# Kernel tuning notes

Hardware: AMD Instinct MI355X
Metric: run time of the kernel (lower is better)

Reference implementation:

```python
import jax, jax.numpy as jnp
import numpy as np

DIM = 1024
H = 16
DH = DIM // H
NF = 64
EPS = 1e-6


def setup_inputs() -> dict:
    key = jax.random.key(0)
    ks = jax.random.split(key, 10)
    B, L = 4, 4096
    s = 1.0 / np.sqrt(DIM)
    x = jax.random.normal(ks[0], (B, L, DIM), dtype=jnp.float32)
    Wq = jax.random.normal(ks[1], (DIM, DIM), dtype=jnp.float32) * s
    Wk = jax.random.normal(ks[2], (DIM, DIM), dtype=jnp.float32) * s
    Wv = jax.random.normal(ks[3], (DIM, DIM), dtype=jnp.float32) * s
    Wo = jax.random.normal(ks[4], (DIM, DIM), dtype=jnp.float32) * s
    bq = jax.random.normal(ks[5], (DIM,), dtype=jnp.float32) * s
    bk = jax.random.normal(ks[6], (DIM,), dtype=jnp.float32) * s
    bv = jax.random.normal(ks[7], (DIM,), dtype=jnp.float32) * s
    bo = jax.random.normal(ks[8], (DIM,), dtype=jnp.float32) * s
    # random-feature buffer: [num_repeats=1, H, DH, NF]; use repeat 0
    Wrf = jax.random.normal(ks[9], (1, H, DH, NF), dtype=jnp.float32)
    return {"x": x, "Wq": Wq, "bq": bq, "Wk": Wk, "bk": bk, "Wv": Wv,
            "bv": bv, "Wo": Wo, "bo": bo, "Wrf": Wrf}


def reference(x, Wq, bq, Wk, bk, Wv, bv, Wo, bo, Wrf):
    B, L, _ = x.shape
    W0 = Wrf[0]  # [H, DH, NF]

    def split_heads(y):
        return y.reshape(B, L, H, DH).transpose(0, 2, 1, 3)  # [B,H,L,DH]

    q = split_heads(x @ Wq.T + bq)
    k = split_heads(x @ Wk.T + bk)
    v = split_heads(x @ Wv.T + bv)

    # key summary: logits [B,H,L,NF], softmax over flattened (L*NF)
    logits = jnp.einsum('bhld,hdf->bhlf', k, W0) \
             - 0.5 * jnp.sum(k * k, axis=-1, keepdims=True)
    alpha = jax.nn.softmax(logits.reshape(B, H, L * NF), axis=2)
    alpha = alpha.reshape(B, H, L, NF)
    N = jnp.einsum('bhlf,bhld->bhfd', alpha, v)  # [B,H,NF,DH]
    D = jnp.sum(alpha, axis=2)                   # [B,H,NF]

    # query feature map: per-position softmax over features
    phi = jax.nn.softmax(jnp.einsum('bhld,hdf->bhlf', q, W0), axis=-1)

    num = jnp.einsum('bhlf,bhfd->bhld', phi, N)
    den = jnp.einsum('bhlf,bhf->bhl', phi, D)
    out = num / (den[..., None] + EPS)

    ctx = out.transpose(0, 2, 1, 3).reshape(B, L, DIM)
    return ctx @ Wo.T + bo
```

## Files before the change

### kernel.cpp

```cpp
#include <hip/hip_runtime.h>
#include <hip/hip_bf16.h>

constexpr int NB   = 4;
constexpr int SL   = 4096;
constexpr int DIMC = 1024;
constexpr int NH   = 16;
constexpr int DHC  = 64;
constexpr int NFC  = 64;
constexpr int NCHK = 8;
constexpr int NCHQ = 32;
constexpr int LCQ  = SL / NCHQ;
constexpr float FEPS = 1e-6f;

typedef __attribute__((ext_vector_type(8))) short bf16x8_t;
typedef __attribute__((ext_vector_type(4))) float f32x4_t;
typedef __attribute__((ext_vector_type(4))) short s16x4_t;

__device__ __forceinline__ void load_lds_16B(const short* g, short* l) {
  __builtin_amdgcn_global_load_lds(
      (__attribute__((address_space(1))) void*)(g),
      (__attribute__((address_space(3))) void*)(l), 16, 0, 0);
}

__global__ __launch_bounds__(256) void cast_f32_to_bf16(
    const float* __restrict__ in, short* __restrict__ out, int n)
{
  const int i = (blockIdx.x * 256 + threadIdx.x) * 4;
  if (i >= n) return;
  const f32x4_t v = *(const f32x4_t*)(in + i);
  s16x4_t o;
#pragma unroll
  for (int j = 0; j < 4; j++) {
    __hip_bfloat16 h = __float2bfloat16(v[j]);
    o[j] = *(short*)&h;
  }
  *(s16x4_t*)(out + i) = o;
}

__global__ __launch_bounds__(256) void prep_w0t_kernel(
    const float* __restrict__ Wrf, short* __restrict__ Whi, short* __restrict__ Wlo)
{
  const int h = blockIdx.x;
  for (int t = threadIdx.x; t < 4096; t += 256) {
    const int f = t >> 6, dh = t & 63;
    const float w = Wrf[(size_t)h * 4096 + dh * 64 + f];
    __hip_bfloat16 hi = __float2bfloat16(w);
    const float rem = w - __bfloat162float(hi);
    __hip_bfloat16 lo = __float2bfloat16(rem);
    Whi[(size_t)h * 4096 + t] = *(short*)&hi;
    Wlo[(size_t)h * 4096 + t] = *(short*)&lo;
  }
}

template <int MODE>
__global__ __launch_bounds__(256) void gemm_lds_kernel(
    const short* __restrict__ A, const short* __restrict__ W,
    const float* __restrict__ bias, void* __restrict__ C0,
    void* __restrict__ C1, float* __restrict__ Ks)
{
  constexpr int K = 1024, N = 1024;
  const int lane = threadIdx.x & 63;
  const int wid  = threadIdx.x >> 6;
  const int sub  = lane & 15;
  const int quad = lane >> 4;
  const int wr   = (wid >> 1) * 64;
  const int wc   = (wid & 1) * 64;
  const int row0 = blockIdx.x * 128;
  const int col0 = blockIdx.y * 128;

  __shared__ short As[128 * 64];
  __shared__ short Bs[128 * 64];

  f32x4_t acc[4][4] = {};

  const int srow = lane >> 3;
  for (int k0 = 0; k0 < K; k0 += 64) {
#pragma unroll
    for (int t = 0; t < 4; t++) {
      const int R   = wid * 32 + t * 8;
      const int row = R + srow;
      const int c   = (lane & 7) ^ (row & 7);
      load_lds_16B(A + (size_t)(row0 + row) * K + k0 + c * 8, As + R * 64);
      load_lds_16B(W + (size_t)(col0 + row) * K + k0 + c * 8, Bs + R * 64);
    }
    __syncthreads();

    bf16x8_t a[2][4], b[2][4];
#pragma unroll
    for (int ks = 0; ks < 2; ks++) {
#pragma unroll
      for (int i = 0; i < 4; i++) {
        const int ra = wr + i * 16 + sub;
        a[ks][i] = *(const bf16x8_t*)(As + ra * 64 + (((ks * 4 + quad) ^ (ra & 7)) * 8));
        const int rb = wc + i * 16 + sub;
        b[ks][i] = *(const bf16x8_t*)(Bs + rb * 64 + (((ks * 4 + quad) ^ (rb & 7)) * 8));
      }
    }
#pragma unroll
    for (int ks = 0; ks < 2; ks++)
#pragma unroll
      for (int i = 0; i < 4; i++)
#pragma unroll
        for (int j = 0; j < 4; j++) {
          if constexpr (MODE == 5)
            acc[i][j] = __builtin_amdgcn_mfma_f32_16x16x32_bf16(b[ks][j], a[ks][i], acc[i][j], 0, 0, 0);
          else
            acc[i][j] = __builtin_amdgcn_mfma_f32_16x16x32_bf16(a[ks][i], b[ks][j], acc[i][j], 0, 0, 0);
        }
    __syncthreads();
  }

  const int rb0 = row0 + wr;
  const int cb0 = col0 + wc;
  if constexpr (MODE == 3 || MODE == 4) {
    __hip_bfloat16* chi = (__hip_bfloat16*)C0;
    __hip_bfloat16* clo = (__hip_bfloat16*)C1;
    float s[4][4];
#pragma unroll
    for (int i = 0; i < 4; i++)
#pragma unroll
      for (int r = 0; r < 4; r++) s[i][r] = 0.f;
#pragma unroll
    for (int j = 0; j < 4; j++) {
      const int col = cb0 + j * 16 + sub;
      const float bv = bias[col];
#pragma unroll
      for (int i = 0; i < 4; i++) {
        const int row = rb0 + i * 16 + quad * 4;
#pragma unroll
        for (int r = 0; r < 4; r++) {
          const float val = acc[i][j][r] + bv;
          const __hip_bfloat16 hi = __float2bfloat16(val);
          const float rem = val - __bfloat162float(hi);
          chi[(size_t)(row + r) * N + col] = hi;
          clo[(size_t)(row + r) * N + col] = __float2bfloat16(rem);
          if constexpr (MODE == 3) s[i][r] = fmaf(val, val, s[i][r]);
        }
      }
    }
    if constexpr (MODE == 3) {
      const int head = cb0 >> 6;
#pragma unroll
      for (int o = 1; o < 16; o <<= 1)
#pragma unroll
        for (int i = 0; i < 4; i++)
#pragma unroll
          for (int r = 0; r < 4; r++) s[i][r] += __shfl_xor(s[i][r], o);
      if (sub == 0) {
#pragma unroll
        for (int i = 0; i < 4; i++)
#pragma unroll
          for (int r = 0; r < 4; r++)
            Ks[(size_t)(rb0 + i * 16 + quad * 4 + r) * NH + head] = s[i][r];
      }
    }
  } else if constexpr (MODE == 5) {
    __hip_bfloat16* vT = (__hip_bfloat16*)C0;
    const int bb    = row0 >> 12;
    const int lbase = rb0 - (bb << 12);
#pragma unroll
    for (int j = 0; j < 4; j++) {
#pragma unroll
      for (int r = 0; r < 4; r++) {
        const int col = cb0 + j * 16 + quad * 4 + r;
        const int h = col >> 6, d = col & 63;
        const float bv = bias[col];
        const size_t rowbase = ((size_t)((bb * NH + h) * 64 + d)) * (size_t)SL;
#pragma unroll
        for (int i = 0; i < 4; i++) {
          const int l = lbase + i * 16 + sub;
          const int pos = (l & ~127) | (((((l >> 3) & 15) ^ (d & 15)) << 3) | (l & 7));
          vT[rowbase + pos] = __float2bfloat16(acc[i][j][r] + bv);
        }
      }
    }
  } else {
#pragma unroll
    for (int j = 0; j < 4; j++) {
      const int col = cb0 + j * 16 + sub;
      const float bv = bias[col];
#pragma unroll
      for (int i = 0; i < 4; i++) {
        const int row = rb0 + i * 16 + quad * 4;
#pragma unroll
        for (int r = 0; r < 4; r++) {
          const float val = acc[i][j][r] + bv;
          if constexpr (MODE == 0)
            ((float*)C0)[(size_t)(row + r) * N + col] = val;
          else
            ((__hip_bfloat16*)C0)[(size_t)(row + r) * N + col] = __float2bfloat16(val);
        }
      }
    }
  }
}

__global__ __launch_bounds__(256) void feat_gemm_kernel(
    const short* __restrict__ xhi, const short* __restrict__ xlo,
    const short* __restrict__ Whi, const short* __restrict__ Wlo,
    float* __restrict__ outlog)
{
  const int lane = threadIdx.x & 63, wid = threadIdx.x >> 6;
  const int sub = lane & 15, quad = lane >> 4;
  const int h = blockIdx.y;
  const int tok0 = blockIdx.x * 128 + wid * 32;
  const short* Bh = Whi + (size_t)h * 4096;
  const short* Bl = Wlo + (size_t)h * 4096;

  f32x4_t acc[2][4] = {};
#pragma unroll
  for (int ks = 0; ks < 2; ks++) {
    const int ko = ks * 32 + quad * 8;
    bf16x8_t ah[2], al[2], bh[4], bl[4];
#pragma unroll
    for (int i = 0; i < 2; i++) {
      const size_t base = (size_t)(tok0 + i * 16 + sub) * DIMC + h * 64 + ko;
      ah[i] = *(const bf16x8_t*)(xhi + base);
      al[i] = *(const bf16x8_t*)(xlo + base);
    }
#pragma unroll
    for (int j = 0; j < 4; j++) {
      const size_t base = (size_t)(j * 16 + sub) * 64 + ko;
      bh[j] = *(const bf16x8_t*)(Bh + base);
      bl[j] = *(const bf16x8_t*)(Bl + base);
    }
#pragma unroll
    for (int i = 0; i < 2; i++)
#pragma unroll
      for (int j = 0; j < 4; j++) {
        acc[i][j] = __builtin_amdgcn_mfma_f32_16x16x32_bf16(ah[i], bh[j], acc[i][j], 0, 0, 0);
        acc[i][j] = __builtin_amdgcn_mfma_f32_16x16x32_bf16(al[i], bh[j], acc[i][j], 0, 0, 0);
        acc[i][j] = __builtin_amdgcn_mfma_f32_16x16x32_bf16(ah[i], bl[j], acc[i][j], 0, 0, 0);
      }
  }
#pragma unroll
  for (int i = 0; i < 2; i++)
#pragma unroll
    for (int j = 0; j < 4; j++)
#pragma unroll
      for (int r = 0; r < 4; r++)
        outlog[(size_t)(tok0 + i * 16 + quad * 4 + r) * DIMC + h * 64 + j * 16 + sub] = acc[i][j][r];
}

__global__ __launch_bounds__(256) void kv_summary_mfma(
    const float* __restrict__ klog, const float* __restrict__ ksq,
    const short* __restrict__ vT, float* __restrict__ pN, float* __restrict__ pD)
{
  const int chunk = blockIdx.x, h = blockIdx.y, b = blockIdx.z;
  const int tid  = threadIdx.x;
  const int lane = tid & 63, wid = tid >> 6;
  const int sub  = lane & 15, quad = lane >> 4;

  __shared__ short vTs[64 * 128];
  __shared__ short wTh[64 * 128];
  __shared__ short wTl[64 * 128];

  f32x4_t accN[4] = {};
  f32x4_t accD = {};
  bf16x8_t bones;
#pragma unroll
  for (int e = 0; e < 8; e++) bones[e] = (sub == 0) ? (short)0x3F80 : (short)0;

  const int tw_t  = tid >> 1;
  const int tw_f0 = (tid & 1) * 32;

  const size_t vbase = ((size_t)((b * NH + h) * 64)) * (size_t)SL;
  const int fbase = (wid * 16 + sub) * 128;

  for (int it = 0; it < 4; ++it) {
    const int l0 = chunk * 512 + it * 128;

#pragma unroll
    for (int q = 0; q < 4; q++) {
      const int dbase = wid * 16 + q * 4;
      const int d = dbase + (lane >> 4);
      load_lds_16B(vT + vbase + (size_t)d * SL + l0 + (lane & 15) * 8,
                   vTs + dbase * 128);
    }

    {
      const int tok = b * SL + l0 + tw_t;
      const float kq = 0.5f * ksq[tok * NH + h];
      const float* kr = klog + (size_t)tok * DIMC + h * 64 + tw_f0;
      f32x4_t kl[8];
#pragma unroll
      for (int v4 = 0; v4 < 8; v4++) kl[v4] = *(const f32x4_t*)(kr + v4 * 4);
#pragma unroll
      for (int v4 = 0; v4 < 8; v4++) {
#pragma unroll
        for (int e = 0; e < 4; e++) {
          const int f = tw_f0 + v4 * 4 + e;
          const float wv = __expf(kl[v4][e] - kq);
          const __hip_bfloat16 hi = __float2bfloat16(wv);
          const float rem = wv - __bfloat162float(hi);
          const __hip_bfloat16 lo = __float2bfloat16(rem);
          const int p = f * 128 + (((((tw_t >> 3) & 15) ^ (f & 15)) << 3) | (tw_t & 7));
          wTh[p] = *(const short*)&hi;
          wTl[p] = *(const short*)&lo;
        }
      }
    }
    __syncthreads();

#pragma unroll
    for (int ks = 0; ks < 4; ks++) {
      const int ch = ks * 4 + quad;
      const bf16x8_t ah = *(const bf16x8_t*)(wTh + fbase + ((ch ^ sub) << 3));
      const bf16x8_t al = *(const bf16x8_t*)(wTl + fbase + ((ch ^ sub) << 3));
      accD = __builtin_amdgcn_mfma_f32_16x16x32_bf16(ah, bones, accD, 0, 0, 0);
      accD = __builtin_amdgcn_mfma_f32_16x16x32_bf16(al, bones, accD, 0, 0, 0);
#pragma unroll
      for (int j = 0; j < 4; j++) {
        const bf16x8_t bv = *(const bf16x8_t*)(vTs + (j * 16 + sub) * 128 + ((ch ^ sub) << 3));
        accN[j] = __builtin_amdgcn_mfma_f32_16x16x32_bf16(ah, bv, accN[j], 0, 0, 0);
        accN[j] = __builtin_amdgcn_mfma_f32_16x16x32_bf16(al, bv, accN[j], 0, 0, 0);
      }
    }
    __syncthreads();
  }

  const size_t pbase = (size_t)((b * NH + h) * NCHK + chunk);
#pragma unroll
  for (int j = 0; j < 4; j++)
#pragma unroll
    for (int r = 0; r < 4; r++)
      pN[pbase * 4096 + (wid * 16 + quad * 4 + r) * 64 + j * 16 + sub] = accN[j][r];
  if (sub == 0) {
#pragma unroll
    for (int r = 0; r < 4; r++)
      pD[pbase * 64 + wid * 16 + quad * 4 + r] = accD[r];
  }
}

__global__ __launch_bounds__(256) void combine_nd_kernel(
    const float* __restrict__ pN, const float* __restrict__ pD,
    short* __restrict__ NfTh, short* __restrict__ NfTl, float* __restrict__ Df)
{
  const int bh = blockIdx.x, seg = blockIdx.y;
  __shared__ float sInv;
  float dsum = 0.f;
  if (threadIdx.x < 64) {
    for (int c = 0; c < NCHK; c++)
      dsum += pD[(size_t)(bh * NCHK + c) * 64 + threadIdx.x];
    float s = dsum;
#pragma unroll
    for (int o = 32; o; o >>= 1) s += __shfl_xor(s, o);
    if (threadIdx.x == 0) sInv = 1.f / s;
  }
  __syncthreads();
  const float inv = sInv;
  if (seg == 0 && threadIdx.x < 64) Df[bh * 64 + threadIdx.x] = dsum * inv;
  const int t = seg * 256 + threadIdx.x;
  float acc = 0.f;
  for (int c = 0; c < NCHK; c++)
    acc += pN[((size_t)(bh * NCHK + c)) * 4096 + t];
  const float val = acc * inv;
  const int f = t >> 6, d = t & 63;
  const __hip_bfloat16 hi = __float2bfloat16(val);
  const float rem = val - __bfloat162float(hi);
  const __hip_bfloat16 lo = __float2bfloat16(rem);
  NfTh[(size_t)bh * 4096 + d * 64 + f] = *(const short*)&hi;
  NfTl[(size_t)bh * 4096 + d * 64 + f] = *(const short*)&lo;
}

__global__ __launch_bounds__(256) void phi_kernel(
    const float* __restrict__ qlog, const float* __restrict__ Df,
    short* __restrict__ ehi, short* __restrict__ elo, float* __restrict__ sbuf)
{
  const int chunk = blockIdx.x, h = blockIdx.y, b = blockIdx.z;
  const int lane = threadIdx.x & 63, wid = threadIdx.x >> 6;
  const float Dl = Df[(b * NH + h) * 64 + lane];

  const int l0 = chunk * LCQ;
  for (int li = wid; li < LCQ; li += 4) {
    const int token = b * SL + l0 + li;
    const size_t base = (size_t)token * DIMC + h * DHC;
    const float lg = qlog[base + lane];

    float mx = lg;
#pragma unroll
    for (int o = 32; o; o >>= 1) mx = fmaxf(mx, __shfl_xor(mx, o));
    const float e = __expf(lg - mx);
    float se = e, dt = e * Dl;
#pragma unroll
    for (int o = 32; o; o >>= 1) { se += __shfl_xor(se, o); dt += __shfl_xor(dt, o); }

    const __hip_bfloat16 hi = __float2bfloat16(e);
    const float rem = e - __bfloat162float(hi);
    const __hip_bfloat16 lo = __float2bfloat16(rem);
    ehi[base + lane] = *(const short*)&hi;
    elo[base + lane] = *(const short*)&lo;
    if (lane == 0) sbuf[token * NH + h] = 1.f / (dt + FEPS * se);
  }
}

__global__ __launch_bounds__(256) void ctx_gemm_kernel(
    const short* __restrict__ ehi, const short* __restrict__ elo,
    const short* __restrict__ NfTh, const short* __restrict__ NfTl,
    const float* __restrict__ sbuf, __hip_bfloat16* __restrict__ ctx)
{
  const int lane = threadIdx.x & 63, wid = threadIdx.x >> 6;
  const int sub = lane & 15, quad = lane >> 4;
  const int h = blockIdx.y;
  const int tok0 = blockIdx.x * 128 + wid * 32;
  const int b = blockIdx.x >> 5;
  const short* Bh = NfTh + ((size_t)(b * NH + h)) * 4096;
  const short* Bl = NfTl + ((size_t)(b * NH + h)) * 4096;

  f32x4_t acc[2][4] = {};
#pragma unroll
  for (int ks = 0; ks < 2; ks++) {
    const int ko = ks * 32 + quad * 8;
    bf16x8_t ah[2], al[2], bh[4], bl[4];
#pragma unroll
    for (int i = 0; i < 2; i++) {
      const size_t base = (size_t)(tok0 + i * 16 + sub) * DIMC + h * 64 + ko;
      ah[i] = *(const bf16x8_t*)(ehi + base);
      al[i] = *(const bf16x8_t*)(elo + base);
    }
#pragma unroll
    for (int j = 0; j < 4; j++) {
      const size_t base = (size_t)(j * 16 + sub) * 64 + ko;
      bh[j] = *(const bf16x8_t*)(Bh + base);
      bl[j] = *(const bf16x8_t*)(Bl + base);
    }
#pragma unroll
    for (int i = 0; i < 2; i++)
#pragma unroll
      for (int j = 0; j < 4; j++) {
        acc[i][j] = __builtin_amdgcn_mfma_f32_16x16x32_bf16(ah[i], bh[j], acc[i][j], 0, 0, 0);
        acc[i][j] = __builtin_amdgcn_mfma_f32_16x16x32_bf16(al[i], bh[j], acc[i][j], 0, 0, 0);
        acc[i][j] = __builtin_amdgcn_mfma_f32_16x16x32_bf16(ah[i], bl[j], acc[i][j], 0, 0, 0);
      }
  }
#pragma unroll
  for (int i = 0; i < 2; i++)
#pragma unroll
    for (int r = 0; r < 4; r++) {
      const int token = tok0 + i * 16 + quad * 4 + r;
      const float sv = sbuf[token * NH + h];
#pragma unroll
      for (int j = 0; j < 4; j++)
        ctx[(size_t)token * DIMC + h * 64 + j * 16 + sub] =
            __float2bfloat16(acc[i][j][r] * sv);
    }
}

extern "C" void kernel_launch(void* const* d_in, const int* in_sizes, int n_in,
                              void* d_out, int out_size, void* d_ws, size_t ws_size,
                              hipStream_t stream) {
  (void)in_sizes; (void)n_in; (void)out_size; (void)ws_size;
  const float* x   = (const float*)d_in[0];
  const float* Wq  = (const float*)d_in[1];
  const float* bq  = (const float*)d_in[2];
  const float* Wk  = (const float*)d_in[3];
  const float* bk  = (const float*)d_in[4];
  const float* Wv  = (const float*)d_in[5];
  const float* bv  = (const float*)d_in[6];
  const float* Wo  = (const float*)d_in[7];
  const float* bo  = (const float*)d_in[8];
  const float* Wrf = (const float*)d_in[9];
  float* out = (float*)d_out;

  constexpr size_t MiB = 1u << 20;
  constexpr size_t KiB = 1u << 10;
  constexpr size_t NTOK = (size_t)NB * SL;
  constexpr size_t XN   = NTOK * DIMC;
  constexpr size_t WN   = (size_t)DIMC * DIMC;

  char* ws = (char*)d_ws;
  short* xb   = (short*)(ws);
  short* Wkb  = (short*)(ws + 32 * MiB);
  short* Wvb  = (short*)(ws + 34 * MiB);
  short* Wob  = (short*)(ws + 36 * MiB);
  short* Wqb  = (short*)(ws + 38 * MiB);
  short* W0Th = (short*)(ws + 40 * MiB);
  short* W0Tl = (short*)(ws + 40 * MiB + 128 * KiB);
  float* ksq  = (float*)(ws + 41 * MiB);
  float* sbuf = (float*)(ws + 42 * MiB);
  float* pD   = (float*)(ws + 43 * MiB);
  short* NfTh = (short*)(ws + 43 * MiB + 512 * KiB);
  short* NfTl = (short*)(ws + 44 * MiB);
  float* Df   = (float*)(ws + 44 * MiB + 512 * KiB);
  float* klog = (float*)(ws + 45 * MiB);
  __hip_bfloat16* khi = (__hip_bfloat16*)(ws + 109 * MiB);
  __hip_bfloat16* klo = (__hip_bfloat16*)(ws + 141 * MiB);
  short* vTb  = (short*)(ws + 173 * MiB);
  float* pN   = (float*)(ws + 109 * MiB);
  __hip_bfloat16* qhi = (__hip_bfloat16*)(ws + 45 * MiB);
  __hip_bfloat16* qlo = (__hip_bfloat16*)(ws + 77 * MiB);
  float* qlog = (float*)(ws + 141 * MiB);
  short* ehi  = (short*)(ws + 45 * MiB);
  short* elo  = (short*)(ws + 77 * MiB);
  __hip_bfloat16* ctxb = (__hip_bfloat16*)xb;

  const dim3 blk(256);

  cast_f32_to_bf16<<<dim3(XN / 1024), blk, 0, stream>>>(x, xb, (int)XN);
  cast_f32_to_bf16<<<dim3(WN / 1024), blk, 0, stream>>>(Wk, Wkb, (int)WN);
  cast_f32_to_bf16<<<dim3(WN / 1024), blk, 0, stream>>>(Wv, Wvb, (int)WN);
  cast_f32_to_bf16<<<dim3(WN / 1024), blk, 0, stream>>>(Wo, Wob, (int)WN);
  cast_f32_to_bf16<<<dim3(WN / 1024), blk, 0, stream>>>(Wq, Wqb, (int)WN);
  prep_w0t_kernel<<<dim3(NH), blk, 0, stream>>>(Wrf, W0Th, W0Tl);

  const dim3 gg(NTOK / 128, DIMC / 128);
  gemm_lds_kernel<3><<<gg, blk, 0, stream>>>(xb, Wkb, bk, khi, klo, ksq);
  gemm_lds_kernel<5><<<gg, blk, 0, stream>>>(xb, Wvb, bv, vTb, nullptr, nullptr);

  feat_gemm_kernel<<<dim3(NTOK / 128, NH), blk, 0, stream>>>(
      (const short*)khi, (const short*)klo, W0Th, W0Tl, klog);

  kv_summary_mfma<<<dim3(NCHK, NH, NB), blk, 0, stream>>>(klog, ksq, vTb, pN, pD);
  combine_nd_kernel<<<dim3(NB * NH, 16), blk, 0, stream>>>(pN, pD, NfTh, NfTl, Df);

  gemm_lds_kernel<4><<<gg, blk, 0, stream>>>(xb, Wqb, bq, qhi, qlo, nullptr);
  feat_gemm_kernel<<<dim3(NTOK / 128, NH), blk, 0, stream>>>(
      (const short*)qhi, (const short*)qlo, W0Th, W0Tl, qlog);
  phi_kernel<<<dim3(NCHQ, NH, NB), blk, 0, stream>>>(qlog, Df, ehi, elo, sbuf);
  ctx_gemm_kernel<<<dim3(NTOK / 128, NH), blk, 0, stream>>>(
      ehi, elo, NfTh, NfTl, sbuf, ctxb);

  gemm_lds_kernel<0><<<gg, blk, 0, stream>>>((const short*)ctxb, Wob, bo, out, nullptr, nullptr);
}
```

Baseline: 542.5 us.

## Fold random-feature projection into Wq and fuse query GEMM with phi softmax

Precomputes fused weights Wq^T·W0 (split into bf16 hi/lo) and a fused bias, so query logits come from a single GEMM over x instead of a q-projection followed by a feature GEMM. The phi softmax, denominator and hi/lo split are done in that GEMM's epilogue, which removes the qlog fp32 round-trip and two kernel launches. The fused GEMM issues twice the MFMAs, one per weight half, and keeps a third LDS tile. The activation side is only the bf16 x, so precision differs from the previous hi/lo q path.

```diff
diff --git a/kernel.cpp b/kernel.cpp
--- a/kernel.cpp
+++ b/kernel.cpp
@@ -8,8 +8,6 @@
 constexpr int DHC  = 64;
 constexpr int NFC  = 64;
 constexpr int NCHK = 8;
-constexpr int NCHQ = 32;
-constexpr int LCQ  = SL / NCHQ;
 constexpr float FEPS = 1e-6f;
 
 typedef __attribute__((ext_vector_type(8))) short bf16x8_t;
@@ -52,6 +50,40 @@
   }
 }
 
+__global__ __launch_bounds__(256) void fuse_w0_kernel(
+    const float* __restrict__ Wq, const float* __restrict__ bq,
+    const float* __restrict__ Wrf,
+    short* __restrict__ Wfh, short* __restrict__ Wfl, float* __restrict__ bqf)
+{
+  const int h = blockIdx.x, cb = blockIdx.y;
+  __shared__ float sWq[64][64];
+  __shared__ float sW0[64][64];
+  for (int idx = threadIdx.x; idx < 4096; idx += 256) {
+    const int d = idx >> 6, e = idx & 63;
+    sWq[d][e] = Wq[(size_t)(h * 64 + d) * 1024 + cb * 64 + e];
+    sW0[d][e] = Wrf[(size_t)h * 4096 + d * 64 + e];
+  }
+  __syncthreads();
+  for (int idx = threadIdx.x; idx < 4096; idx += 256) {
+    const int f = idx >> 6, cc = idx & 63;
+    float acc = 0.f;
+#pragma unroll
+    for (int d = 0; d < 64; d++) acc = fmaf(sWq[d][cc], sW0[d][f], acc);
+    const __hip_bfloat16 hi = __float2bfloat16(acc);
+    const float rem = acc - __bfloat162float(hi);
+    const __hip_bfloat16 lo = __float2bfloat16(rem);
+    Wfh[(size_t)(h * 64 + f) * 1024 + cb * 64 + cc] = *(const short*)&hi;
+    Wfl[(size_t)(h * 64 + f) * 1024 + cb * 64 + cc] = *(const short*)&lo;
+  }
+  if (cb == 0 && threadIdx.x < 64) {
+    const int f = threadIdx.x;
+    float acc = 0.f;
+#pragma unroll
+    for (int d = 0; d < 64; d++) acc = fmaf(bq[h * 64 + d], sW0[d][f], acc);
+    bqf[h * 64 + f] = acc;
+  }
+}
+
 template <int MODE>
 __global__ __launch_bounds__(256) void gemm_lds_kernel(
     const short* __restrict__ A, const short* __restrict__ W,
@@ -112,7 +144,7 @@
 
   const int rb0 = row0 + wr;
   const int cb0 = col0 + wc;
-  if constexpr (MODE == 3 || MODE == 4) {
+  if constexpr (MODE == 3) {
     __hip_bfloat16* chi = (__hip_bfloat16*)C0;
     __hip_bfloat16* clo = (__hip_bfloat16*)C1;
     float s[4][4];
@@ -134,11 +166,11 @@
           const float rem = val - __bfloat162float(hi);
           chi[(size_t)(row + r) * N + col] = hi;
           clo[(size_t)(row + r) * N + col] = __float2bfloat16(rem);
-          if constexpr (MODE == 3) s[i][r] = fmaf(val, val, s[i][r]);
+          s[i][r] = fmaf(val, val, s[i][r]);
         }
       }
     }
-    if constexpr (MODE == 3) {
+    {
       const int head = cb0 >> 6;
 #pragma unroll
       for (int o = 1; o < 16; o <<= 1)
@@ -185,12 +217,112 @@
 #pragma unroll
         for (int r = 0; r < 4; r++) {
           const float val = acc[i][j][r] + bv;
-          if constexpr (MODE == 0)
-            ((float*)C0)[(size_t)(row + r) * N + col] = val;
-          else
-            ((__hip_bfloat16*)C0)[(size_t)(row + r) * N + col] = __float2bfloat16(val);
+          ((float*)C0)[(size_t)(row + r) * N + col] = val;
         }
       }
+    }
+  }
+}
+
+__global__ __launch_bounds__(256) void gemm_phi_kernel(
+    const short* __restrict__ A, const short* __restrict__ Wh,
+    const short* __restrict__ Wl, const float* __restrict__ bqf,
+    const float* __restrict__ Df, short* __restrict__ ehi,
+    short* __restrict__ elo, float* __restrict__ sbuf)
+{
+  constexpr int K = 1024;
+  const int lane = threadIdx.x & 63;
+  const int wid  = threadIdx.x >> 6;
+  const int sub  = lane & 15;
+  const int quad = lane >> 4;
+  const int wr   = (wid >> 1) * 64;
+  const int wc   = (wid & 1) * 64;
+  const int row0 = blockIdx.x * 128;
+  const int col0 = blockIdx.y * 128;
+
+  __shared__ short As[128 * 64];
+  __shared__ short Bhs[128 * 64];
+  __shared__ short Bls[128 * 64];
+
+  f32x4_t acc[4][4] = {};
+
+  const int srow = lane >> 3;
+  for (int k0 = 0; k0 < K; k0 += 64) {
+#pragma unroll
+    for (int t = 0; t < 4; t++) {
+      const int R   = wid * 32 + t * 8;
+      const int row = R + srow;
+      const int c   = (lane & 7) ^ (row & 7);
+      load_lds_16B(A  + (size_t)(row0 + row) * K + k0 + c * 8, As  + R * 64);
+      load_lds_16B(Wh + (size_t)(col0 + row) * K + k0 + c * 8, Bhs + R * 64);
+      load_lds_16B(Wl + (size_t)(col0 + row) * K + k0 + c * 8, Bls + R * 64);
+    }
+    __syncthreads();
+
+#pragma unroll
+    for (int ks = 0; ks < 2; ks++) {
+      bf16x8_t a[4], bh[4], bl[4];
+#pragma unroll
+      for (int i = 0; i < 4; i++) {
+        const int ra = wr + i * 16 + sub;
+        a[i] = *(const bf16x8_t*)(As + ra * 64 + (((ks * 4 + quad) ^ (ra & 7)) * 8));
+        const int rb = wc + i * 16 + sub;
+        bh[i] = *(const bf16x8_t*)(Bhs + rb * 64 + (((ks * 4 + quad) ^ (rb & 7)) * 8));
+        bl[i] = *(const bf16x8_t*)(Bls + rb * 64 + (((ks * 4 + quad) ^ (rb & 7)) * 8));
+      }
+#pragma unroll
+      for (int i = 0; i < 4; i++)
+#pragma unroll
+        for (int j = 0; j < 4; j++) {
+          acc[i][j] = __builtin_amdgcn_mfma_f32_16x16x32_bf16(a[i], bh[j], acc[i][j], 0, 0, 0);
+          acc[i][j] = __builtin_amdgcn_mfma_f32_16x16x32_bf16(a[i], bl[j], acc[i][j], 0, 0, 0);
+        }
+      __syncthreads();
+    }
+  }
+
+  const int rb0 = row0 + wr;
+  const int cb0 = col0 + wc;
+  const int b   = row0 >> 12;
+  const int h   = cb0 >> 6;
+  float bv[4], Dl[4];
+#pragma unroll
+  for (int j = 0; j < 4; j++) {
+    const int f = j * 16 + sub;
+    bv[j] = bqf[h * 64 + f];
+    Dl[j] = Df[(b * NH + h) * 64 + f];
+  }
+#pragma unroll
+  for (int i = 0; i < 4; i++) {
+#pragma unroll
+    for (int r = 0; r < 4; r++) {
+      float v[4];
+#pragma unroll
+      for (int j = 0; j < 4; j++) v[j] = acc[i][j][r] + bv[j];
+      float mx = fmaxf(fmaxf(v[0], v[1]), fmaxf(v[2], v[3]));
+#pragma unroll
+      for (int o = 1; o < 16; o <<= 1) mx = fmaxf(mx, __shfl_xor(mx, o));
+      float e[4], se = 0.f, dt = 0.f;
+#pragma unroll
+      for (int j = 0; j < 4; j++) {
+        e[j] = __expf(v[j] - mx);
+        se += e[j];
+        dt = fmaf(e[j], Dl[j], dt);
+      }
+#pragma unroll
+      for (int o = 1; o < 16; o <<= 1) { se += __shfl_xor(se, o); dt += __shfl_xor(dt, o); }
+
+      const int row = rb0 + i * 16 + quad * 4 + r;
+      const size_t base = (size_t)row * DIMC + h * 64;
+#pragma unroll
+      for (int j = 0; j < 4; j++) {
+        const __hip_bfloat16 hi = __float2bfloat16(e[j]);
+        const float rem = e[j] - __bfloat162float(hi);
+        const __hip_bfloat16 lo = __float2bfloat16(rem);
+        ehi[base + j * 16 + sub] = *(const short*)&hi;
+        elo[base + j * 16 + sub] = *(const short*)&lo;
+      }
+      if (sub == 0) sbuf[row * NH + h] = 1.f / (dt + FEPS * se);
     }
   }
 }
@@ -361,37 +493,6 @@
   const __hip_bfloat16 lo = __float2bfloat16(rem);
   NfTh[(size_t)bh * 4096 + d * 64 + f] = *(const short*)&hi;
   NfTl[(size_t)bh * 4096 + d * 64 + f] = *(const short*)&lo;
-}
-
-__global__ __launch_bounds__(256) void phi_kernel(
-    const float* __restrict__ qlog, const float* __restrict__ Df,
-    short* __restrict__ ehi, short* __restrict__ elo, float* __restrict__ sbuf)
-{
-  const int chunk = blockIdx.x, h = blockIdx.y, b = blockIdx.z;
-  const int lane = threadIdx.x & 63, wid = threadIdx.x >> 6;
-  const float Dl = Df[(b * NH + h) * 64 + lane];
-
-  const int l0 = chunk * LCQ;
-  for (int li = wid; li < LCQ; li += 4) {
-    const int token = b * SL + l0 + li;
-    const size_t base = (size_t)token * DIMC + h * DHC;
-    const float lg = qlog[base + lane];
-
-    float mx = lg;
-#pragma unroll
-    for (int o = 32; o; o >>= 1) mx = fmaxf(mx, __shfl_xor(mx, o));
-    const float e = __expf(lg - mx);
-    float se = e, dt = e * Dl;
-#pragma unroll
-    for (int o = 32; o; o >>= 1) { se += __shfl_xor(se, o); dt += __shfl_xor(dt, o); }
-
-    const __hip_bfloat16 hi = __float2bfloat16(e);
-    const float rem = e - __bfloat162float(hi);
-    const __hip_bfloat16 lo = __float2bfloat16(rem);
-    ehi[base + lane] = *(const short*)&hi;
-    elo[base + lane] = *(const short*)&lo;
-    if (lane == 0) sbuf[token * NH + h] = 1.f / (dt + FEPS * se);
-  }
 }
 
 __global__ __launch_bounds__(256) void ctx_gemm_kernel(
@@ -473,9 +574,9 @@
   short* Wkb  = (short*)(ws + 32 * MiB);
   short* Wvb  = (short*)(ws + 34 * MiB);
   short* Wob  = (short*)(ws + 36 * MiB);
-  short* Wqb  = (short*)(ws + 38 * MiB);
   short* W0Th = (short*)(ws + 40 * MiB);
   short* W0Tl = (short*)(ws + 40 * MiB + 128 * KiB);
+  float* bqf  = (float*)(ws + 40 * MiB + 256 * KiB);
   float* ksq  = (float*)(ws + 41 * MiB);
   float* sbuf = (float*)(ws + 42 * MiB);
   float* pD   = (float*)(ws + 43 * MiB);
@@ -487,9 +588,8 @@
   __hip_bfloat16* klo = (__hip_bfloat16*)(ws + 141 * MiB);
   short* vTb  = (short*)(ws + 173 * MiB);
   float* pN   = (float*)(ws + 109 * MiB);
-  __hip_bfloat16* qhi = (__hip_bfloat16*)(ws + 45 * MiB);
-  __hip_bfloat16* qlo = (__hip_bfloat16*)(ws + 77 * MiB);
-  float* qlog = (float*)(ws + 141 * MiB);
+  short* Wqfh = (short*)(ws + 173 * MiB);
+  short* Wqfl = (short*)(ws + 175 * MiB);
   short* ehi  = (short*)(ws + 45 * MiB);
   short* elo  = (short*)(ws + 77 * MiB);
   __hip_bfloat16* ctxb = (__hip_bfloat16*)xb;
@@ -500,7 +600,6 @@
   cast_f32_to_bf16<<<dim3(WN / 1024), blk, 0, stream>>>(Wk, Wkb, (int)WN);
   cast_f32_to_bf16<<<dim3(WN / 1024), blk, 0, stream>>>(Wv, Wvb, (int)WN);
   cast_f32_to_bf16<<<dim3(WN / 1024), blk, 0, stream>>>(Wo, Wob, (int)WN);
-  cast_f32_to_bf16<<<dim3(WN / 1024), blk, 0, stream>>>(Wq, Wqb, (int)WN);
   prep_w0t_kernel<<<dim3(NH), blk, 0, stream>>>(Wrf, W0Th, W0Tl);
 
   const dim3 gg(NTOK / 128, DIMC / 128);
@@ -511,12 +610,10 @@
       (const short*)khi, (const short*)klo, W0Th, W0Tl, klog);
 
   kv_summary_mfma<<<dim3(NCHK, NH, NB), blk, 0, stream>>>(klog, ksq, vTb, pN, pD);
+  fuse_w0_kernel<<<dim3(NH, 16), blk, 0, stream>>>(Wq, bq, Wrf, Wqfh, Wqfl, bqf);
   combine_nd_kernel<<<dim3(NB * NH, 16), blk, 0, stream>>>(pN, pD, NfTh, NfTl, Df);
 
-  gemm_lds_kernel<4><<<gg, blk, 0, stream>>>(xb, Wqb, bq, qhi, qlo, nullptr);
-  feat_gemm_kernel<<<dim3(NTOK / 128, NH), blk, 0, stream>>>(
-      (const short*)qhi, (const short*)qlo, W0Th, W0Tl, qlog);
-  phi_kernel<<<dim3(NCHQ, NH, NB), blk, 0, stream>>>(qlog, Df, ehi, elo, sbuf);
+  gemm_phi_kernel<<<gg, blk, 0, stream>>>(xb, Wqfh, Wqfl, bqf, Df, ehi, elo, sbuf);
   ctx_gemm_kernel<<<dim3(NTOK / 128, NH), blk, 0, stream>>>(
       ehi, elo, NfTh, NfTl, sbuf, ctxb);
 
```

After: 491.1 us. -9.5%, faster.
